# Kernel optimization log

Measured on AMD Instinct MI355X. Metric: run time of the kernel, lower is better.

Reference implementation:

```python
import jax, jax.numpy as jnp
import numpy as np

B, N = 64, 16384
EPS_RT = 1e-06  # recovery_time epsilon from the torch code


def _init_params(key):
    ks = jax.random.split(key, 10)
    s = 0.1
    p = {}
    # ContextEncoder: 4 -> 16 -> 8 -> 1 (hidden_dim=8, first layer hidden*2)
    p['ctx_W1'] = jax.random.normal(ks[0], (4, 16), jnp.float32) * s
    p['ctx_b1'] = jnp.zeros((16,), jnp.float32)
    p['ctx_W2'] = jax.random.normal(ks[1], (16, 8), jnp.float32) * s
    p['ctx_b2'] = jnp.zeros((8,), jnp.float32)
    p['ctx_W3'] = jax.random.normal(ks[2], (8, 1), jnp.float32) * s
    p['ctx_b3'] = jnp.zeros((1,), jnp.float32)
    # RiskPropagationNetwork: 4 -> 64 -> 32 -> 16 -> 1
    p['p_W1'] = jax.random.normal(ks[3], (4, 64), jnp.float32) * s
    p['p_b1'] = jnp.zeros((64,), jnp.float32)
    p['p_W2'] = jax.random.normal(ks[4], (64, 32), jnp.float32) * s
    p['p_b2'] = jnp.zeros((32,), jnp.float32)
    p['p_W3'] = jax.random.normal(ks[5], (32, 16), jnp.float32) * s
    p['p_b3'] = jnp.zeros((16,), jnp.float32)
    p['p_Wo'] = jax.random.normal(ks[6], (16, 1), jnp.float32) * s
    p['p_bo'] = jnp.zeros((1,), jnp.float32)
    # learned scalar risk-component weights
    p['w_threat'] = jnp.float32(0.4)
    p['w_impact'] = jnp.float32(0.3)
    p['w_vuln'] = jnp.float32(0.2)
    p['w_ctx'] = jnp.float32(0.1)
    return p


def setup_inputs() -> dict:
    key = jax.random.key(0)
    ks = jax.random.split(key, 12)
    inp = {
        'threat_predictions': jax.random.normal(ks[0], (B, N), jnp.float32),
        'criticality': jax.random.uniform(ks[1], (B, N), jnp.float32),
        'connectivity': jax.random.uniform(ks[2], (B, N), jnp.float32),
        'sensitivity': jax.random.uniform(ks[3], (B, N), jnp.float32),
        'business_value': jax.random.uniform(ks[4], (B, N), jnp.float32),
        'data_sensitivity': jax.random.uniform(ks[5], (B, N), jnp.float32),
        'compliance_requirements': jax.random.uniform(ks[6], (B, N), jnp.float32),
        'recovery_time': jax.random.uniform(ks[7], (B, N), jnp.float32),
        'severity': jax.random.uniform(ks[8], (B, N), jnp.float32) * 10.0,
    }
    inp.update(_init_params(ks[9]))
    return inp


def _forward(threat_predictions, criticality, connectivity, sensitivity,
             business_value, data_sensitivity, compliance_requirements,
             recovery_time, severity,
             ctx_W1, ctx_b1, ctx_W2, ctx_b2, ctx_W3, ctx_b3,
             p_W1, p_b1, p_W2, p_b2, p_W3, p_b3, p_Wo, p_bo,
             w_threat, w_impact, w_vuln, w_ctx):
    # --- risk components ---
    threat_risk = jax.nn.sigmoid(threat_predictions * 3.0)
    m = jnp.max(criticality)
    impact_risk = jnp.where(m > 0, criticality / jnp.maximum(m, 1e-12), criticality)
    vuln_risk = severity / 10.0
    # ContextEncoder: concat 4 context scalars -> MLP -> sigmoid
    ctx_in = jnp.stack([business_value, data_sensitivity, compliance_requirements,
                        1.0 / (recovery_time + EPS_RT)], axis=-1)  # [B,N,4]
    h = jax.nn.relu(ctx_in @ ctx_W1 + ctx_b1)
    h = jax.nn.relu(h @ ctx_W2 + ctx_b2)
    context_risk = jax.nn.sigmoid((h @ ctx_W3 + ctx_b3)[..., 0])
    # --- weighted combination with normalized learned weights ---
    total_w = w_threat + w_impact + w_vuln + w_ctx
    base_risk = (w_threat * threat_risk + w_impact * impact_risk
                 + w_vuln * vuln_risk + w_ctx * context_risk) / total_w
    # --- RiskPropagationNetwork (dropout is identity in eval) ---
    feats = jnp.stack([base_risk, criticality, connectivity, sensitivity], axis=-1)  # [B,N,4]
    x = jax.nn.relu(feats @ p_W1 + p_b1)
    x = jax.nn.relu(x @ p_W2 + p_b2)
    x = jax.nn.relu(x @ p_W3 + p_b3)
    return jax.nn.sigmoid((x @ p_Wo + p_bo)[..., 0])  # [B,N]


def reference(threat_predictions, criticality, connectivity, sensitivity,
              business_value, data_sensitivity, compliance_requirements,
              recovery_time, severity,
              ctx_W1, ctx_b1, ctx_W2, ctx_b2, ctx_W3, ctx_b3,
              p_W1, p_b1, p_W2, p_b2, p_W3, p_b3, p_Wo, p_bo,
              w_threat, w_impact, w_vuln, w_ctx):
    return _forward(threat_predictions, criticality, connectivity, sensitivity,
                    business_value, data_sensitivity, compliance_requirements,
                    recovery_time, severity,
                    ctx_W1, ctx_b1, ctx_W2, ctx_b2, ctx_W3, ctx_b3,
                    p_W1, p_b1, p_W2, p_b2, p_W3, p_b3, p_Wo, p_bo,
                    w_threat, w_impact, w_vuln, w_ctx)
```

## Files before the change

kernel.cpp:

```cpp
#include <hip/hip_runtime.h>
#include <hip/hip_bf16.h>

typedef short bf16x8 __attribute__((ext_vector_type(8)));
typedef float f32x4 __attribute__((ext_vector_type(4)));
typedef unsigned int uint;

#define TOTAL (64 * 16384)
#define BLOCKS (TOTAL / 256)
#define MAXBLOCKS 256

#define WS_PART(ws) ((float*)(ws))
#define WS_SCAL(ws) ((float*)((char*)(ws) + 2048))
#define WS_FRAG(ws) ((uint4*)((char*)(ws) + 4096))

__device__ __forceinline__ uint bf16rne(float x) {
    uint b = __float_as_uint(x);
    return (b + 0x7fffu + ((b >> 16) & 1u)) >> 16;
}
__device__ __forceinline__ short bf16s(float x) { return (short)bf16rne(x); }
__device__ __forceinline__ uint pk2(float lo, float hi) {
    __hip_bfloat162 h2 = __float22bfloat162_rn(make_float2(lo, hi));
    uint u;
    __builtin_memcpy(&u, &h2, sizeof(u));
    return u;
}
__device__ __forceinline__ float relu_(float x) { return fmaxf(x, 0.0f); }
__device__ __forceinline__ float fast_sigmoid(float x) {
    return __builtin_amdgcn_rcpf(1.0f + __expf(-x));
}
__device__ __forceinline__ float dot4r(f32x4 v, float4 w) {
    return fmaf(relu_(v[0]), w.x, fmaf(relu_(v[1]), w.y,
           fmaf(relu_(v[2]), w.z, relu_(v[3]) * w.w)));
}
__device__ __forceinline__ bf16x8 u4bf(uint4 u) {
    bf16x8 r;
    __builtin_memcpy(&r, &u, sizeof(r));
    return r;
}
__device__ __forceinline__ uint4 bfu4(bf16x8 f) {
    uint4 u;
    __builtin_memcpy(&u, &f, sizeof(u));
    return u;
}
__device__ __forceinline__ uint4 f4u4(float4 f) {
    uint4 u;
    __builtin_memcpy(&u, &f, sizeof(u));
    return u;
}

__global__ __launch_bounds__(256) void crit_max_kernel(
        const float* __restrict__ crit, float* __restrict__ part, int n4) {
    __shared__ float smax[4];
    const int tid = threadIdx.x;
    float m = 0.0f;
    const float4* c4 = (const float4*)crit;
    for (int i = blockIdx.x * 256 + tid; i < n4; i += gridDim.x * 256) {
        float4 v = c4[i];
        m = fmaxf(fmaxf(m, v.x), fmaxf(fmaxf(v.y, v.z), v.w));
    }
#pragma unroll
    for (int off = 32; off > 0; off >>= 1)
        m = fmaxf(m, __shfl_xor(m, off));
    if ((tid & 63) == 0) smax[tid >> 6] = m;
    __syncthreads();
    if (tid == 0)
        part[blockIdx.x] = fmaxf(fmaxf(smax[0], smax[1]), fmaxf(smax[2], smax[3]));
}

__global__ __launch_bounds__(64) void prep_kernel(
        const float* __restrict__ pW1,  const float* __restrict__ pb1,
        const float* __restrict__ pW2,  const float* __restrict__ pb2,
        const float* __restrict__ pW3,  const float* __restrict__ pb3,
        const float* __restrict__ pWo,  const float* __restrict__ pbo,
        const float* __restrict__ w_threat, const float* __restrict__ w_impact,
        const float* __restrict__ w_vuln,   const float* __restrict__ w_ctx,
        void* __restrict__ ws) {
    const int lane = threadIdx.x;
    const int g    = lane >> 4;
    const int c    = lane & 15;
    const bf16x8 z8 = {0,0,0,0,0,0,0,0};

    {
        const float* part = WS_PART(ws);
        float4 pm4 = ((const float4*)part)[lane];
        float pm = fmaxf(fmaxf(pm4.x, pm4.y), fmaxf(pm4.z, pm4.w));
#pragma unroll
        for (int off = 32; off > 0; off >>= 1)
            pm = fmaxf(pm, __shfl_xor(pm, off));
        if (lane == 0) {
            float wt = w_threat[0], wi = w_impact[0], wv = w_vuln[0], wc = w_ctx[0];
            float inv_tw = 1.0f / (wt + wi + wv + wc);
            float* scal = WS_SCAL(ws);
            scal[0] = wt * inv_tw;
            scal[1] = wi * inv_tw;
            scal[2] = wv * inv_tw;
            scal[3] = wc * inv_tw;
            scal[4] = (pm > 0.0f) ? 1.0f / fmaxf(pm, 1e-12f) : 1.0f;
            scal[5] = pbo[0];
            scal[6] = 0.0f;
            scal[7] = 0.0f;
        }
    }

    uint4* fr = WS_FRAG(ws);
#pragma unroll
    for (int nt = 0; nt < 4; ++nt) {
        bf16x8 f = z8;
        f[0] = bf16s(pW1[nt * 16 + c]);
        f[4] = bf16s(pb1[nt * 16 + c]);
        f[5] = bf16s(pW1[64 + nt * 16 + c]);
        f[6] = bf16s(pW1[128 + nt * 16 + c]);
        f[7] = bf16s(pW1[192 + nt * 16 + c]);
        fr[nt * 64 + lane] = bfu4(f);
    }
#pragma unroll
    for (int mt = 0; mt < 2; ++mt)
#pragma unroll
        for (int kf = 0; kf < 2; ++kf) {
            bf16x8 f;
#pragma unroll
            for (int i = 0; i < 4; ++i)
                f[i] = bf16s(pW2[(kf * 32 + 4 * g + i) * 32 + mt * 16 + c]);
#pragma unroll
            for (int i = 4; i < 8; ++i)
                f[i] = bf16s(pW2[(kf * 32 + 16 + 4 * g + (i - 4)) * 32 + mt * 16 + c]);
            fr[(4 + mt * 2 + kf) * 64 + lane] = bfu4(f);
        }
    {
        bf16x8 f;
#pragma unroll
        for (int i = 0; i < 4; ++i) f[i] = bf16s(pW3[(4 * g + i) * 16 + c]);
#pragma unroll
        for (int i = 4; i < 8; ++i) f[i] = bf16s(pW3[(16 + 4 * g + (i - 4)) * 16 + c]);
        fr[8 * 64 + lane] = bfu4(f);
    }
    fr[9  * 64 + lane] = f4u4(((const float4*)pb2)[g]);
    fr[10 * 64 + lane] = f4u4(((const float4*)pb2)[4 + g]);
    fr[11 * 64 + lane] = f4u4(((const float4*)pb3)[g]);
    fr[12 * 64 + lane] = f4u4(((const float4*)pWo)[g]);
}

__global__ __launch_bounds__(256, 4) void risk_mfma_kernel(
        const float* __restrict__ tp,   const float* __restrict__ crit,
        const float* __restrict__ conn, const float* __restrict__ sens,
        const float* __restrict__ bv,   const float* __restrict__ dsv,
        const float* __restrict__ comp, const float* __restrict__ rt,
        const float* __restrict__ sev,
        const float* __restrict__ ctxW1, const float* __restrict__ ctxb1,
        const float* __restrict__ ctxW2, const float* __restrict__ ctxb2,
        const float* __restrict__ ctxW3, const float* __restrict__ ctxb3,
        const void* __restrict__ ws,
        float* __restrict__ out) {
    const int lane = threadIdx.x & 63;
    const int g    = lane >> 4;
    const f32x4 z4 = {0.f,0.f,0.f,0.f};

    const float* scal = WS_SCAL(ws);
    const float wtn = scal[0], win = scal[1], wvn = scal[2], wcn = scal[3];
    const float imul = scal[4], pbo0 = scal[5];

    const uint4* fr = WS_FRAG(ws);
    bf16x8 w1All[4];
#pragma unroll
    for (int nt = 0; nt < 4; ++nt) w1All[nt] = u4bf(fr[nt * 64 + lane]);
    bf16x8 w2A[2][2];
#pragma unroll
    for (int mt = 0; mt < 2; ++mt)
#pragma unroll
        for (int kf = 0; kf < 2; ++kf)
            w2A[mt][kf] = u4bf(fr[(4 + mt * 2 + kf) * 64 + lane]);
    bf16x8 w3A = u4bf(fr[8 * 64 + lane]);
    f32x4 b2i[2], b3i;
    float4 wog;
    __builtin_memcpy(&b2i[0], &fr[9  * 64 + lane], 16);
    __builtin_memcpy(&b2i[1], &fr[10 * 64 + lane], 16);
    __builtin_memcpy(&b3i,    &fr[11 * 64 + lane], 16);
    __builtin_memcpy(&wog,    &fr[12 * 64 + lane], 16);

    const int e = blockIdx.x * 256 + (int)threadIdx.x;

    float tpv = tp[e], cv = crit[e], cnv = conn[e], snv = sens[e];
    float bvv = bv[e], dvv = dsv[e], cpv = comp[e], rtv = rt[e], svv = sev[e];

    float invrt = __builtin_amdgcn_rcpf(rtv + 1e-6f);
    float h1[16];
#pragma unroll
    for (int j = 0; j < 16; ++j) {
        float a = ctxb1[j];
        a = fmaf(bvv,   ctxW1[j],      a);
        a = fmaf(dvv,   ctxW1[16 + j], a);
        a = fmaf(cpv,   ctxW1[32 + j], a);
        a = fmaf(invrt, ctxW1[48 + j], a);
        h1[j] = fmaxf(a, 0.0f);
    }
    float h2[8];
#pragma unroll
    for (int k = 0; k < 8; ++k) h2[k] = ctxb2[k];
#pragma unroll
    for (int j = 0; j < 16; ++j)
#pragma unroll
        for (int k = 0; k < 8; ++k)
            h2[k] = fmaf(h1[j], ctxW2[j * 8 + k], h2[k]);
    float a3 = ctxb3[0];
#pragma unroll
    for (int k = 0; k < 8; ++k)
        a3 = fmaf(fmaxf(h2[k], 0.0f), ctxW3[k], a3);
    float ctxr = fast_sigmoid(a3);

    float threat = fast_sigmoid(3.0f * tpv);
    float impact = cv * imul;
    float vuln   = svv * 0.1f;
    float base   = fmaf(wcn, ctxr,
                   fmaf(wtn, threat, fmaf(win, impact, wvn * vuln)));

    uint bb = bf16rne(base);
    uint zc = pk2(1.0f, cv);
    uint wc2 = pk2(cnv, snv);
    float pv[4];
#pragma unroll
    for (int t = 0; t < 4; ++t) {
        bool sel = (g == t);
        uint4 pB;
        pB.x = sel ? bb  : 0u;
        pB.y = 0u;
        pB.z = sel ? zc  : 0u;
        pB.w = sel ? wc2 : 0u;
        bf16x8 bp = u4bf(pB);
        uint l1p[4][2];
#pragma unroll
        for (int nt = 0; nt < 4; ++nt) {
            f32x4 c1 = __builtin_amdgcn_mfma_f32_16x16x32_bf16(w1All[nt], bp, z4, 0, 0, 0);
            l1p[nt][0] = pk2(relu_(c1[0]), relu_(c1[1]));
            l1p[nt][1] = pk2(relu_(c1[2]), relu_(c1[3]));
        }
        uint4 B0 = make_uint4(l1p[0][0], l1p[0][1], l1p[1][0], l1p[1][1]);
        uint4 B1 = make_uint4(l1p[2][0], l1p[2][1], l1p[3][0], l1p[3][1]);
        bf16x8 b0 = u4bf(B0), b1 = u4bf(B1);
        uint l2p[2][2];
#pragma unroll
        for (int mt = 0; mt < 2; ++mt) {
            f32x4 acc = __builtin_amdgcn_mfma_f32_16x16x32_bf16(w2A[mt][0], b0, b2i[mt], 0, 0, 0);
            f32x4 c2  = __builtin_amdgcn_mfma_f32_16x16x32_bf16(w2A[mt][1], b1, acc, 0, 0, 0);
            l2p[mt][0] = pk2(relu_(c2[0]), relu_(c2[1]));
            l2p[mt][1] = pk2(relu_(c2[2]), relu_(c2[3]));
        }
        uint4 B3 = make_uint4(l2p[0][0], l2p[0][1], l2p[1][0], l2p[1][1]);
        f32x4 c3 = __builtin_amdgcn_mfma_f32_16x16x32_bf16(w3A, u4bf(B3), b3i, 0, 0, 0);
        pv[t] = dot4r(c3, wog);
    }
#pragma unroll
    for (int t = 0; t < 4; ++t) {
        pv[t] += __shfl_xor(pv[t], 16);
        pv[t] += __shfl_xor(pv[t], 32);
    }
    float psel = (g == 0) ? pv[0] : (g == 1) ? pv[1] : (g == 2) ? pv[2] : pv[3];
    out[e] = fast_sigmoid(psel + pbo0);
}

extern "C" void kernel_launch(void* const* d_in, const int* in_sizes, int n_in,
                              void* d_out, int out_size, void* d_ws, size_t ws_size,
                              hipStream_t stream) {
    const float* tp    = (const float*)d_in[0];
    const float* crit  = (const float*)d_in[1];
    const float* conn  = (const float*)d_in[2];
    const float* sens  = (const float*)d_in[3];
    const float* bv    = (const float*)d_in[4];
    const float* dsv   = (const float*)d_in[5];
    const float* comp  = (const float*)d_in[6];
    const float* rt    = (const float*)d_in[7];
    const float* sev   = (const float*)d_in[8];
    const float* ctxW1 = (const float*)d_in[9];
    const float* ctxb1 = (const float*)d_in[10];
    const float* ctxW2 = (const float*)d_in[11];
    const float* ctxb2 = (const float*)d_in[12];
    const float* ctxW3 = (const float*)d_in[13];
    const float* ctxb3 = (const float*)d_in[14];
    const float* pW1   = (const float*)d_in[15];
    const float* pb1   = (const float*)d_in[16];
    const float* pW2   = (const float*)d_in[17];
    const float* pb2   = (const float*)d_in[18];
    const float* pW3   = (const float*)d_in[19];
    const float* pb3   = (const float*)d_in[20];
    const float* pWo   = (const float*)d_in[21];
    const float* pbo   = (const float*)d_in[22];
    const float* w_t   = (const float*)d_in[23];
    const float* w_i   = (const float*)d_in[24];
    const float* w_v   = (const float*)d_in[25];
    const float* w_c   = (const float*)d_in[26];

    float* out = (float*)d_out;

    crit_max_kernel<<<MAXBLOCKS, 256, 0, stream>>>(crit, WS_PART(d_ws), TOTAL / 4);
    prep_kernel<<<1, 64, 0, stream>>>(
        pW1, pb1, pW2, pb2, pW3, pb3, pWo, pbo,
        w_t, w_i, w_v, w_c, d_ws);
    risk_mfma_kernel<<<BLOCKS, 256, 0, stream>>>(
        tp, crit, conn, sens, bv, dsv, comp, rt, sev,
        ctxW1, ctxb1, ctxW2, ctxb2, ctxW3, ctxb3, d_ws, out);
}
```

Measured before the change: 37.60 us.

## Merge crit-max and prep kernels, finish max reduction in main kernel, two iterations per thread

The criticality max-reduction and weight-fragment prep kernels become one launch, with an extra block doing the prep. The final reduction of the 256 partial maxima now happens in every wave of the main kernel, which removes one kernel launch and its serialization point. The main kernel also processes two elements per thread, halving the grid so the fragment and scalar loads are amortized. The cost is redundant partial-max reads and shuffles in every wave, plus less parallelism per launch.

```diff
diff --git a/kernel.cpp b/kernel.cpp
--- a/kernel.cpp
+++ b/kernel.cpp
@@ -6,8 +6,9 @@
 typedef unsigned int uint;
 
 #define TOTAL (64 * 16384)
-#define BLOCKS (TOTAL / 256)
-#define MAXBLOCKS 256
+#define ITERS 2
+#define RBLOCKS (TOTAL / (256 * ITERS))
+#define PBLOCKS 256
 
 #define WS_PART(ws) ((float*)(ws))
 #define WS_SCAL(ws) ((float*)((char*)(ws) + 2048))
@@ -48,58 +49,52 @@
     return u;
 }
 
-__global__ __launch_bounds__(256) void crit_max_kernel(
-        const float* __restrict__ crit, float* __restrict__ part, int n4) {
-    __shared__ float smax[4];
-    const int tid = threadIdx.x;
-    float m = 0.0f;
-    const float4* c4 = (const float4*)crit;
-    for (int i = blockIdx.x * 256 + tid; i < n4; i += gridDim.x * 256) {
-        float4 v = c4[i];
-        m = fmaxf(fmaxf(m, v.x), fmaxf(fmaxf(v.y, v.z), v.w));
-    }
-#pragma unroll
-    for (int off = 32; off > 0; off >>= 1)
-        m = fmaxf(m, __shfl_xor(m, off));
-    if ((tid & 63) == 0) smax[tid >> 6] = m;
-    __syncthreads();
-    if (tid == 0)
-        part[blockIdx.x] = fmaxf(fmaxf(smax[0], smax[1]), fmaxf(smax[2], smax[3]));
-}
-
-__global__ __launch_bounds__(64) void prep_kernel(
+__global__ __launch_bounds__(256) void setup_kernel(
+        const float* __restrict__ crit,
         const float* __restrict__ pW1,  const float* __restrict__ pb1,
         const float* __restrict__ pW2,  const float* __restrict__ pb2,
         const float* __restrict__ pW3,  const float* __restrict__ pb3,
         const float* __restrict__ pWo,  const float* __restrict__ pbo,
         const float* __restrict__ w_threat, const float* __restrict__ w_impact,
         const float* __restrict__ w_vuln,   const float* __restrict__ w_ctx,
-        void* __restrict__ ws) {
+        void* __restrict__ ws, int n4) {
+    if (blockIdx.x < PBLOCKS) {
+        __shared__ float smax[4];
+        const int tid = threadIdx.x;
+        float m = 0.0f;
+        const float4* c4 = (const float4*)crit;
+        for (int i = blockIdx.x * 256 + tid; i < n4; i += PBLOCKS * 256) {
+            float4 v = c4[i];
+            m = fmaxf(fmaxf(m, v.x), fmaxf(fmaxf(v.y, v.z), v.w));
+        }
+#pragma unroll
+        for (int off = 32; off > 0; off >>= 1)
+            m = fmaxf(m, __shfl_xor(m, off));
+        if ((tid & 63) == 0) smax[tid >> 6] = m;
+        __syncthreads();
+        if (tid == 0)
+            WS_PART(ws)[blockIdx.x] =
+                fmaxf(fmaxf(smax[0], smax[1]), fmaxf(smax[2], smax[3]));
+        return;
+    }
+    if (threadIdx.x >= 64) return;
     const int lane = threadIdx.x;
     const int g    = lane >> 4;
     const int c    = lane & 15;
     const bf16x8 z8 = {0,0,0,0,0,0,0,0};
 
-    {
-        const float* part = WS_PART(ws);
-        float4 pm4 = ((const float4*)part)[lane];
-        float pm = fmaxf(fmaxf(pm4.x, pm4.y), fmaxf(pm4.z, pm4.w));
-#pragma unroll
-        for (int off = 32; off > 0; off >>= 1)
-            pm = fmaxf(pm, __shfl_xor(pm, off));
-        if (lane == 0) {
-            float wt = w_threat[0], wi = w_impact[0], wv = w_vuln[0], wc = w_ctx[0];
-            float inv_tw = 1.0f / (wt + wi + wv + wc);
-            float* scal = WS_SCAL(ws);
-            scal[0] = wt * inv_tw;
-            scal[1] = wi * inv_tw;
-            scal[2] = wv * inv_tw;
-            scal[3] = wc * inv_tw;
-            scal[4] = (pm > 0.0f) ? 1.0f / fmaxf(pm, 1e-12f) : 1.0f;
-            scal[5] = pbo[0];
-            scal[6] = 0.0f;
-            scal[7] = 0.0f;
-        }
+    if (lane == 0) {
+        float wt = w_threat[0], wi = w_impact[0], wv = w_vuln[0], wc = w_ctx[0];
+        float inv_tw = 1.0f / (wt + wi + wv + wc);
+        float* scal = WS_SCAL(ws);
+        scal[0] = wt * inv_tw;
+        scal[1] = wi * inv_tw;
+        scal[2] = wv * inv_tw;
+        scal[3] = wc * inv_tw;
+        scal[4] = 0.0f;
+        scal[5] = pbo[0];
+        scal[6] = 0.0f;
+        scal[7] = 0.0f;
     }
 
     uint4* fr = WS_FRAG(ws);
@@ -157,7 +152,17 @@
 
     const float* scal = WS_SCAL(ws);
     const float wtn = scal[0], win = scal[1], wvn = scal[2], wcn = scal[3];
-    const float imul = scal[4], pbo0 = scal[5];
+    const float pbo0 = scal[5];
+
+    float imul;
+    {
+        float4 pm4 = ((const float4*)WS_PART(ws))[lane];
+        float pm = fmaxf(fmaxf(pm4.x, pm4.y), fmaxf(pm4.z, pm4.w));
+#pragma unroll
+        for (int off = 32; off > 0; off >>= 1)
+            pm = fmaxf(pm, __shfl_xor(pm, off));
+        imul = (pm > 0.0f) ? __builtin_amdgcn_rcpf(fmaxf(pm, 1e-12f)) : 1.0f;
+    }
 
     const uint4* fr = WS_FRAG(ws);
     bf16x8 w1All[4];
@@ -177,84 +182,89 @@
     __builtin_memcpy(&b3i,    &fr[11 * 64 + lane], 16);
     __builtin_memcpy(&wog,    &fr[12 * 64 + lane], 16);
 
-    const int e = blockIdx.x * 256 + (int)threadIdx.x;
-
-    float tpv = tp[e], cv = crit[e], cnv = conn[e], snv = sens[e];
-    float bvv = bv[e], dvv = dsv[e], cpv = comp[e], rtv = rt[e], svv = sev[e];
-
-    float invrt = __builtin_amdgcn_rcpf(rtv + 1e-6f);
-    float h1[16];
-#pragma unroll
-    for (int j = 0; j < 16; ++j) {
-        float a = ctxb1[j];
-        a = fmaf(bvv,   ctxW1[j],      a);
-        a = fmaf(dvv,   ctxW1[16 + j], a);
-        a = fmaf(cpv,   ctxW1[32 + j], a);
-        a = fmaf(invrt, ctxW1[48 + j], a);
-        h1[j] = fmaxf(a, 0.0f);
-    }
-    float h2[8];
-#pragma unroll
-    for (int k = 0; k < 8; ++k) h2[k] = ctxb2[k];
-#pragma unroll
-    for (int j = 0; j < 16; ++j)
+    const int eblock = blockIdx.x * (256 * ITERS);
+
+#pragma unroll 1
+    for (int it = 0; it < ITERS; ++it) {
+        const int e = eblock + it * 256 + (int)threadIdx.x;
+
+        float tpv = tp[e], cv = crit[e], cnv = conn[e], snv = sens[e];
+        float bvv = bv[e], dvv = dsv[e], cpv = comp[e], rtv = rt[e], svv = sev[e];
+
+        float invrt = __builtin_amdgcn_rcpf(rtv + 1e-6f);
+        float h1[16];
+#pragma unroll
+        for (int j = 0; j < 16; ++j) {
+            float a = ctxb1[j];
+            a = fmaf(bvv,   ctxW1[j],      a);
+            a = fmaf(dvv,   ctxW1[16 + j], a);
+            a = fmaf(cpv,   ctxW1[32 + j], a);
+            a = fmaf(invrt, ctxW1[48 + j], a);
+            h1[j] = fmaxf(a, 0.0f);
+        }
+        float h2[8];
+#pragma unroll
+        for (int k = 0; k < 8; ++k) h2[k] = ctxb2[k];
+#pragma unroll
+        for (int j = 0; j < 16; ++j)
+#pragma unroll
+            for (int k = 0; k < 8; ++k)
+                h2[k] = fmaf(h1[j], ctxW2[j * 8 + k], h2[k]);
+        float a3 = ctxb3[0];
 #pragma unroll
         for (int k = 0; k < 8; ++k)
-            h2[k] = fmaf(h1[j], ctxW2[j * 8 + k], h2[k]);
-    float a3 = ctxb3[0];
-#pragma unroll
-    for (int k = 0; k < 8; ++k)
-        a3 = fmaf(fmaxf(h2[k], 0.0f), ctxW3[k], a3);
-    float ctxr = fast_sigmoid(a3);
-
-    float threat = fast_sigmoid(3.0f * tpv);
-    float impact = cv * imul;
-    float vuln   = svv * 0.1f;
-    float base   = fmaf(wcn, ctxr,
-                   fmaf(wtn, threat, fmaf(win, impact, wvn * vuln)));
-
-    uint bb = bf16rne(base);
-    uint zc = pk2(1.0f, cv);
-    uint wc2 = pk2(cnv, snv);
-    float pv[4];
-#pragma unroll
-    for (int t = 0; t < 4; ++t) {
-        bool sel = (g == t);
-        uint4 pB;
-        pB.x = sel ? bb  : 0u;
-        pB.y = 0u;
-        pB.z = sel ? zc  : 0u;
-        pB.w = sel ? wc2 : 0u;
-        bf16x8 bp = u4bf(pB);
-        uint l1p[4][2];
-#pragma unroll
-        for (int nt = 0; nt < 4; ++nt) {
-            f32x4 c1 = __builtin_amdgcn_mfma_f32_16x16x32_bf16(w1All[nt], bp, z4, 0, 0, 0);
-            l1p[nt][0] = pk2(relu_(c1[0]), relu_(c1[1]));
-            l1p[nt][1] = pk2(relu_(c1[2]), relu_(c1[3]));
-        }
-        uint4 B0 = make_uint4(l1p[0][0], l1p[0][1], l1p[1][0], l1p[1][1]);
-        uint4 B1 = make_uint4(l1p[2][0], l1p[2][1], l1p[3][0], l1p[3][1]);
-        bf16x8 b0 = u4bf(B0), b1 = u4bf(B1);
-        uint l2p[2][2];
-#pragma unroll
-        for (int mt = 0; mt < 2; ++mt) {
-            f32x4 acc = __builtin_amdgcn_mfma_f32_16x16x32_bf16(w2A[mt][0], b0, b2i[mt], 0, 0, 0);
-            f32x4 c2  = __builtin_amdgcn_mfma_f32_16x16x32_bf16(w2A[mt][1], b1, acc, 0, 0, 0);
-            l2p[mt][0] = pk2(relu_(c2[0]), relu_(c2[1]));
-            l2p[mt][1] = pk2(relu_(c2[2]), relu_(c2[3]));
-        }
-        uint4 B3 = make_uint4(l2p[0][0], l2p[0][1], l2p[1][0], l2p[1][1]);
-        f32x4 c3 = __builtin_amdgcn_mfma_f32_16x16x32_bf16(w3A, u4bf(B3), b3i, 0, 0, 0);
-        pv[t] = dot4r(c3, wog);
-    }
-#pragma unroll
-    for (int t = 0; t < 4; ++t) {
-        pv[t] += __shfl_xor(pv[t], 16);
-        pv[t] += __shfl_xor(pv[t], 32);
-    }
-    float psel = (g == 0) ? pv[0] : (g == 1) ? pv[1] : (g == 2) ? pv[2] : pv[3];
-    out[e] = fast_sigmoid(psel + pbo0);
+            a3 = fmaf(fmaxf(h2[k], 0.0f), ctxW3[k], a3);
+        float ctxr = fast_sigmoid(a3);
+
+        float threat = fast_sigmoid(3.0f * tpv);
+        float impact = cv * imul;
+        float vuln   = svv * 0.1f;
+        float base   = fmaf(wcn, ctxr,
+                       fmaf(wtn, threat, fmaf(win, impact, wvn * vuln)));
+
+        uint bb  = bf16rne(base);
+        uint zc  = pk2(1.0f, cv);
+        uint wc2 = pk2(cnv, snv);
+        float pv[4];
+#pragma unroll
+        for (int t = 0; t < 4; ++t) {
+            bool sel = (g == t);
+            uint4 pB;
+            pB.x = sel ? bb  : 0u;
+            pB.y = 0u;
+            pB.z = sel ? zc  : 0u;
+            pB.w = sel ? wc2 : 0u;
+            bf16x8 bp = u4bf(pB);
+            uint l1p[4][2];
+#pragma unroll
+            for (int nt = 0; nt < 4; ++nt) {
+                f32x4 c1 = __builtin_amdgcn_mfma_f32_16x16x32_bf16(w1All[nt], bp, z4, 0, 0, 0);
+                l1p[nt][0] = pk2(relu_(c1[0]), relu_(c1[1]));
+                l1p[nt][1] = pk2(relu_(c1[2]), relu_(c1[3]));
+            }
+            uint4 B0 = make_uint4(l1p[0][0], l1p[0][1], l1p[1][0], l1p[1][1]);
+            uint4 B1 = make_uint4(l1p[2][0], l1p[2][1], l1p[3][0], l1p[3][1]);
+            bf16x8 b0 = u4bf(B0), b1 = u4bf(B1);
+            uint l2p[2][2];
+#pragma unroll
+            for (int mt = 0; mt < 2; ++mt) {
+                f32x4 acc = __builtin_amdgcn_mfma_f32_16x16x32_bf16(w2A[mt][0], b0, b2i[mt], 0, 0, 0);
+                f32x4 c2  = __builtin_amdgcn_mfma_f32_16x16x32_bf16(w2A[mt][1], b1, acc, 0, 0, 0);
+                l2p[mt][0] = pk2(relu_(c2[0]), relu_(c2[1]));
+                l2p[mt][1] = pk2(relu_(c2[2]), relu_(c2[3]));
+            }
+            uint4 B3 = make_uint4(l2p[0][0], l2p[0][1], l2p[1][0], l2p[1][1]);
+            f32x4 c3 = __builtin_amdgcn_mfma_f32_16x16x32_bf16(w3A, u4bf(B3), b3i, 0, 0, 0);
+            pv[t] = dot4r(c3, wog);
+        }
+#pragma unroll
+        for (int t = 0; t < 4; ++t) {
+            pv[t] += __shfl_xor(pv[t], 16);
+            pv[t] += __shfl_xor(pv[t], 32);
+        }
+        float psel = (g == 0) ? pv[0] : (g == 1) ? pv[1] : (g == 2) ? pv[2] : pv[3];
+        out[e] = fast_sigmoid(psel + pbo0);
+    }
 }
 
 extern "C" void kernel_launch(void* const* d_in, const int* in_sizes, int n_in,
@@ -290,11 +300,10 @@
 
     float* out = (float*)d_out;
 
-    crit_max_kernel<<<MAXBLOCKS, 256, 0, stream>>>(crit, WS_PART(d_ws), TOTAL / 4);
-    prep_kernel<<<1, 64, 0, stream>>>(
-        pW1, pb1, pW2, pb2, pW3, pb3, pWo, pbo,
-        w_t, w_i, w_v, w_c, d_ws);
-    risk_mfma_kernel<<<BLOCKS, 256, 0, stream>>>(
+    setup_kernel<<<PBLOCKS + 1, 256, 0, stream>>>(
+        crit, pW1, pb1, pW2, pb2, pW3, pb3, pWo, pbo,
+        w_t, w_i, w_v, w_c, d_ws, TOTAL / 4);
+    risk_mfma_kernel<<<RBLOCKS, 256, 0, stream>>>(
         tp, crit, conn, sens, bv, dsv, comp, rt, sev,
         ctxW1, ctxb1, ctxW2, ctxb2, ctxW3, ctxb3, d_ws, out);
 }
```

After: 44.65 us. +18.8%, slower.

## Switch propagation MLP to 32x32x16 MFMA tiles processing two element groups per wave

Applied to the files above, without the earlier changes.

The propagation MLP moves from 16x16x32 bf16 MFMAs, run as four passes of 16 elements per wave, to 32x32x16 MFMAs run as two passes of 32 elements. Lanes trade inputs with a cross-half shuffle. The prep kernel re-packs the weight, bias and output-weight fragments into the 32x32 operand layout. The aim is to cut the MFMA instruction count, the per-pass packing overhead and the final shuffle reduction. In exchange it uses larger 16-wide accumulators, which raises register pressure, and launch bounds drop from 4 to 3 waves per SIMD.

```diff
diff --git a/kernel.cpp b/kernel.cpp
--- a/kernel.cpp
+++ b/kernel.cpp
@@ -3,6 +3,7 @@
 
 typedef short bf16x8 __attribute__((ext_vector_type(8)));
 typedef float f32x4 __attribute__((ext_vector_type(4)));
+typedef float f32x16 __attribute__((ext_vector_type(16)));
 typedef unsigned int uint;
 
 #define TOTAL (64 * 16384)
@@ -27,10 +28,6 @@
 __device__ __forceinline__ float relu_(float x) { return fmaxf(x, 0.0f); }
 __device__ __forceinline__ float fast_sigmoid(float x) {
     return __builtin_amdgcn_rcpf(1.0f + __expf(-x));
-}
-__device__ __forceinline__ float dot4r(f32x4 v, float4 w) {
-    return fmaf(relu_(v[0]), w.x, fmaf(relu_(v[1]), w.y,
-           fmaf(relu_(v[2]), w.z, relu_(v[3]) * w.w)));
 }
 __device__ __forceinline__ bf16x8 u4bf(uint4 u) {
     bf16x8 r;
@@ -76,8 +73,8 @@
         const float* __restrict__ w_vuln,   const float* __restrict__ w_ctx,
         void* __restrict__ ws) {
     const int lane = threadIdx.x;
-    const int g    = lane >> 4;
-    const int c    = lane & 15;
+    const int h    = lane >> 5;
+    const int q    = lane & 31;
     const bf16x8 z8 = {0,0,0,0,0,0,0,0};
 
     {
@@ -104,43 +101,65 @@
 
     uint4* fr = WS_FRAG(ws);
 #pragma unroll
-    for (int nt = 0; nt < 4; ++nt) {
+    for (int ot = 0; ot < 2; ++ot) {
         bf16x8 f = z8;
-        f[0] = bf16s(pW1[nt * 16 + c]);
-        f[4] = bf16s(pb1[nt * 16 + c]);
-        f[5] = bf16s(pW1[64 + nt * 16 + c]);
-        f[6] = bf16s(pW1[128 + nt * 16 + c]);
-        f[7] = bf16s(pW1[192 + nt * 16 + c]);
-        fr[nt * 64 + lane] = bfu4(f);
-    }
-#pragma unroll
-    for (int mt = 0; mt < 2; ++mt)
-#pragma unroll
-        for (int kf = 0; kf < 2; ++kf) {
-            bf16x8 f;
-#pragma unroll
-            for (int i = 0; i < 4; ++i)
-                f[i] = bf16s(pW2[(kf * 32 + 4 * g + i) * 32 + mt * 16 + c]);
-#pragma unroll
-            for (int i = 4; i < 8; ++i)
-                f[i] = bf16s(pW2[(kf * 32 + 16 + 4 * g + (i - 4)) * 32 + mt * 16 + c]);
-            fr[(4 + mt * 2 + kf) * 64 + lane] = bfu4(f);
-        }
-    {
+        if (h == 0) {
+            f[0] = bf16s(pW1[ot * 32 + q]);
+            f[4] = bf16s(pb1[ot * 32 + q]);
+            f[5] = bf16s(pW1[64 + ot * 32 + q]);
+            f[6] = bf16s(pW1[128 + ot * 32 + q]);
+            f[7] = bf16s(pW1[192 + ot * 32 + q]);
+        }
+        fr[ot * 64 + lane] = bfu4(f);
+    }
+#pragma unroll
+    for (int kf = 0; kf < 4; ++kf) {
         bf16x8 f;
 #pragma unroll
-        for (int i = 0; i < 4; ++i) f[i] = bf16s(pW3[(4 * g + i) * 16 + c]);
-#pragma unroll
-        for (int i = 4; i < 8; ++i) f[i] = bf16s(pW3[(16 + 4 * g + (i - 4)) * 16 + c]);
-        fr[8 * 64 + lane] = bfu4(f);
-    }
-    fr[9  * 64 + lane] = f4u4(((const float4*)pb2)[g]);
-    fr[10 * 64 + lane] = f4u4(((const float4*)pb2)[4 + g]);
-    fr[11 * 64 + lane] = f4u4(((const float4*)pb3)[g]);
-    fr[12 * 64 + lane] = f4u4(((const float4*)pWo)[g]);
-}
-
-__global__ __launch_bounds__(256, 4) void risk_mfma_kernel(
+        for (int i = 0; i < 8; ++i) {
+            int U = 16 * kf + 4 * h + (i & 3) + 8 * (i >> 2);
+            f[i] = bf16s(pW2[U * 32 + q]);
+        }
+        fr[(2 + kf) * 64 + lane] = bfu4(f);
+    }
+#pragma unroll
+    for (int kf = 0; kf < 2; ++kf) {
+        bf16x8 f = z8;
+        if (q < 16) {
+#pragma unroll
+            for (int i = 0; i < 8; ++i) {
+                int U = 16 * kf + 4 * h + (i & 3) + 8 * (i >> 2);
+                f[i] = bf16s(pW3[U * 16 + q]);
+            }
+        }
+        fr[(6 + kf) * 64 + lane] = bfu4(f);
+    }
+#pragma unroll
+    for (int s = 0; s < 4; ++s) {
+        float4 t;
+        t.x = pb2[((4 * s + 0) & 3) + 8 * ((4 * s + 0) >> 2) + 4 * h];
+        t.y = pb2[((4 * s + 1) & 3) + 8 * ((4 * s + 1) >> 2) + 4 * h];
+        t.z = pb2[((4 * s + 2) & 3) + 8 * ((4 * s + 2) >> 2) + 4 * h];
+        t.w = pb2[((4 * s + 3) & 3) + 8 * ((4 * s + 3) >> 2) + 4 * h];
+        fr[(8 + s) * 64 + lane] = f4u4(t);
+    }
+#pragma unroll
+    for (int s = 0; s < 2; ++s) {
+        float4 t3, tw;
+        t3.x = pb3[((4 * s + 0) & 3) + 8 * ((4 * s + 0) >> 2) + 4 * h];
+        t3.y = pb3[((4 * s + 1) & 3) + 8 * ((4 * s + 1) >> 2) + 4 * h];
+        t3.z = pb3[((4 * s + 2) & 3) + 8 * ((4 * s + 2) >> 2) + 4 * h];
+        t3.w = pb3[((4 * s + 3) & 3) + 8 * ((4 * s + 3) >> 2) + 4 * h];
+        tw.x = pWo[((4 * s + 0) & 3) + 8 * ((4 * s + 0) >> 2) + 4 * h];
+        tw.y = pWo[((4 * s + 1) & 3) + 8 * ((4 * s + 1) >> 2) + 4 * h];
+        tw.z = pWo[((4 * s + 2) & 3) + 8 * ((4 * s + 2) >> 2) + 4 * h];
+        tw.w = pWo[((4 * s + 3) & 3) + 8 * ((4 * s + 3) >> 2) + 4 * h];
+        fr[(12 + s) * 64 + lane] = f4u4(t3);
+        fr[(14 + s) * 64 + lane] = f4u4(tw);
+    }
+}
+
+__global__ __launch_bounds__(256, 3) void risk_mfma_kernel(
         const float* __restrict__ tp,   const float* __restrict__ crit,
         const float* __restrict__ conn, const float* __restrict__ sens,
         const float* __restrict__ bv,   const float* __restrict__ dsv,
@@ -152,30 +171,41 @@
         const void* __restrict__ ws,
         float* __restrict__ out) {
     const int lane = threadIdx.x & 63;
-    const int g    = lane >> 4;
-    const f32x4 z4 = {0.f,0.f,0.f,0.f};
+    const int h    = lane >> 5;
 
     const float* scal = WS_SCAL(ws);
     const float wtn = scal[0], win = scal[1], wvn = scal[2], wcn = scal[3];
     const float imul = scal[4], pbo0 = scal[5];
 
     const uint4* fr = WS_FRAG(ws);
-    bf16x8 w1All[4];
-#pragma unroll
-    for (int nt = 0; nt < 4; ++nt) w1All[nt] = u4bf(fr[nt * 64 + lane]);
-    bf16x8 w2A[2][2];
-#pragma unroll
-    for (int mt = 0; mt < 2; ++mt)
-#pragma unroll
-        for (int kf = 0; kf < 2; ++kf)
-            w2A[mt][kf] = u4bf(fr[(4 + mt * 2 + kf) * 64 + lane]);
-    bf16x8 w3A = u4bf(fr[8 * 64 + lane]);
-    f32x4 b2i[2], b3i;
-    float4 wog;
-    __builtin_memcpy(&b2i[0], &fr[9  * 64 + lane], 16);
-    __builtin_memcpy(&b2i[1], &fr[10 * 64 + lane], 16);
-    __builtin_memcpy(&b3i,    &fr[11 * 64 + lane], 16);
-    __builtin_memcpy(&wog,    &fr[12 * 64 + lane], 16);
+    bf16x8 w1A[2], w2A[4], w3A[2];
+#pragma unroll
+    for (int ot = 0; ot < 2; ++ot) w1A[ot] = u4bf(fr[ot * 64 + lane]);
+#pragma unroll
+    for (int kf = 0; kf < 4; ++kf) w2A[kf] = u4bf(fr[(2 + kf) * 64 + lane]);
+#pragma unroll
+    for (int kf = 0; kf < 2; ++kf) w3A[kf] = u4bf(fr[(6 + kf) * 64 + lane]);
+    f32x16 b2i;
+#pragma unroll
+    for (int s = 0; s < 4; ++s) {
+        float4 t;
+        __builtin_memcpy(&t, &fr[(8 + s) * 64 + lane], 16);
+        b2i[4 * s + 0] = t.x; b2i[4 * s + 1] = t.y;
+        b2i[4 * s + 2] = t.z; b2i[4 * s + 3] = t.w;
+    }
+    f32x16 c3i;
+#pragma unroll
+    for (int s = 0; s < 2; ++s) {
+        float4 t;
+        __builtin_memcpy(&t, &fr[(12 + s) * 64 + lane], 16);
+        c3i[4 * s + 0] = t.x; c3i[4 * s + 1] = t.y;
+        c3i[4 * s + 2] = t.z; c3i[4 * s + 3] = t.w;
+    }
+#pragma unroll
+    for (int r = 8; r < 16; ++r) c3i[r] = 0.0f;
+    float4 wo0, wo1;
+    __builtin_memcpy(&wo0, &fr[14 * 64 + lane], 16);
+    __builtin_memcpy(&wo1, &fr[15 * 64 + lane], 16);
 
     const int e = blockIdx.x * 256 + (int)threadIdx.x;
 
@@ -213,48 +243,72 @@
     float base   = fmaf(wcn, ctxr,
                    fmaf(wtn, threat, fmaf(win, impact, wvn * vuln)));
 
-    uint bb = bf16rne(base);
-    uint zc = pk2(1.0f, cv);
-    uint wc2 = pk2(cnv, snv);
-    float pv[4];
-#pragma unroll
-    for (int t = 0; t < 4; ++t) {
-        bool sel = (g == t);
+    uint a0 = bf16rne(base);
+    uint a2 = pk2(1.0f, cv);
+    uint a3u = pk2(cnv, snv);
+    uint s0 = __shfl_xor(a0, 32);
+    uint s2 = __shfl_xor(a2, 32);
+    uint s3 = __shfl_xor(a3u, 32);
+
+    const f32x16 z16 = {0.f,0.f,0.f,0.f,0.f,0.f,0.f,0.f,
+                        0.f,0.f,0.f,0.f,0.f,0.f,0.f,0.f};
+    float ov[2];
+#pragma unroll
+    for (int T = 0; T < 2; ++T) {
         uint4 pB;
-        pB.x = sel ? bb  : 0u;
+        if (T == 0) {
+            pB.x = (h == 0) ? a0  : 0u;
+            pB.z = (h == 0) ? a2  : 0u;
+            pB.w = (h == 0) ? a3u : 0u;
+        } else {
+            pB.x = (h == 0) ? s0  : 0u;
+            pB.z = (h == 0) ? s2  : 0u;
+            pB.w = (h == 0) ? s3  : 0u;
+        }
         pB.y = 0u;
-        pB.z = sel ? zc  : 0u;
-        pB.w = sel ? wc2 : 0u;
         bf16x8 bp = u4bf(pB);
-        uint l1p[4][2];
-#pragma unroll
-        for (int nt = 0; nt < 4; ++nt) {
-            f32x4 c1 = __builtin_amdgcn_mfma_f32_16x16x32_bf16(w1All[nt], bp, z4, 0, 0, 0);
-            l1p[nt][0] = pk2(relu_(c1[0]), relu_(c1[1]));
-            l1p[nt][1] = pk2(relu_(c1[2]), relu_(c1[3]));
-        }
-        uint4 B0 = make_uint4(l1p[0][0], l1p[0][1], l1p[1][0], l1p[1][1]);
-        uint4 B1 = make_uint4(l1p[2][0], l1p[2][1], l1p[3][0], l1p[3][1]);
-        bf16x8 b0 = u4bf(B0), b1 = u4bf(B1);
-        uint l2p[2][2];
-#pragma unroll
-        for (int mt = 0; mt < 2; ++mt) {
-            f32x4 acc = __builtin_amdgcn_mfma_f32_16x16x32_bf16(w2A[mt][0], b0, b2i[mt], 0, 0, 0);
-            f32x4 c2  = __builtin_amdgcn_mfma_f32_16x16x32_bf16(w2A[mt][1], b1, acc, 0, 0, 0);
-            l2p[mt][0] = pk2(relu_(c2[0]), relu_(c2[1]));
-            l2p[mt][1] = pk2(relu_(c2[2]), relu_(c2[3]));
-        }
-        uint4 B3 = make_uint4(l2p[0][0], l2p[0][1], l2p[1][0], l2p[1][1]);
-        f32x4 c3 = __builtin_amdgcn_mfma_f32_16x16x32_bf16(w3A, u4bf(B3), b3i, 0, 0, 0);
-        pv[t] = dot4r(c3, wog);
-    }
-#pragma unroll
-    for (int t = 0; t < 4; ++t) {
-        pv[t] += __shfl_xor(pv[t], 16);
-        pv[t] += __shfl_xor(pv[t], 32);
-    }
-    float psel = (g == 0) ? pv[0] : (g == 1) ? pv[1] : (g == 2) ? pv[2] : pv[3];
-    out[e] = fast_sigmoid(psel + pbo0);
+        f32x16 d1a = __builtin_amdgcn_mfma_f32_32x32x16_bf16(w1A[0], bp, z16, 0, 0, 0);
+        f32x16 d1b = __builtin_amdgcn_mfma_f32_32x32x16_bf16(w1A[1], bp, z16, 0, 0, 0);
+        uint4 B2[4];
+#pragma unroll
+        for (int s = 0; s < 2; ++s) {
+            B2[s].x = pk2(relu_(d1a[8*s+0]), relu_(d1a[8*s+1]));
+            B2[s].y = pk2(relu_(d1a[8*s+2]), relu_(d1a[8*s+3]));
+            B2[s].z = pk2(relu_(d1a[8*s+4]), relu_(d1a[8*s+5]));
+            B2[s].w = pk2(relu_(d1a[8*s+6]), relu_(d1a[8*s+7]));
+            B2[2+s].x = pk2(relu_(d1b[8*s+0]), relu_(d1b[8*s+1]));
+            B2[2+s].y = pk2(relu_(d1b[8*s+2]), relu_(d1b[8*s+3]));
+            B2[2+s].z = pk2(relu_(d1b[8*s+4]), relu_(d1b[8*s+5]));
+            B2[2+s].w = pk2(relu_(d1b[8*s+6]), relu_(d1b[8*s+7]));
+        }
+        f32x16 d2 = b2i;
+#pragma unroll
+        for (int kf = 0; kf < 4; ++kf)
+            d2 = __builtin_amdgcn_mfma_f32_32x32x16_bf16(w2A[kf], u4bf(B2[kf]), d2, 0, 0, 0);
+        uint4 B3[2];
+#pragma unroll
+        for (int s = 0; s < 2; ++s) {
+            B3[s].x = pk2(relu_(d2[8*s+0]), relu_(d2[8*s+1]));
+            B3[s].y = pk2(relu_(d2[8*s+2]), relu_(d2[8*s+3]));
+            B3[s].z = pk2(relu_(d2[8*s+4]), relu_(d2[8*s+5]));
+            B3[s].w = pk2(relu_(d2[8*s+6]), relu_(d2[8*s+7]));
+        }
+        f32x16 d3 = c3i;
+        d3 = __builtin_amdgcn_mfma_f32_32x32x16_bf16(w3A[0], u4bf(B3[0]), d3, 0, 0, 0);
+        d3 = __builtin_amdgcn_mfma_f32_32x32x16_bf16(w3A[1], u4bf(B3[1]), d3, 0, 0, 0);
+        float p = 0.0f;
+        p = fmaf(relu_(d3[0]), wo0.x, p);
+        p = fmaf(relu_(d3[1]), wo0.y, p);
+        p = fmaf(relu_(d3[2]), wo0.z, p);
+        p = fmaf(relu_(d3[3]), wo0.w, p);
+        p = fmaf(relu_(d3[4]), wo1.x, p);
+        p = fmaf(relu_(d3[5]), wo1.y, p);
+        p = fmaf(relu_(d3[6]), wo1.z, p);
+        p = fmaf(relu_(d3[7]), wo1.w, p);
+        p += __shfl_xor(p, 32);
+        ov[T] = fast_sigmoid(p + pbo0);
+    }
+    out[e] = (h == 0) ? ov[0] : ov[1];
 }
 
 extern "C" void kernel_launch(void* const* d_in, const int* in_sizes, int n_in,
```

Result: no change. 37.86 us (+0.7%).
